# Kernel tuning notes

Hardware: AMD Instinct MI355X
Metric: run time of the kernel (lower is better)

Reference implementation:

```python
import jax, jax.numpy as jnp
import numpy as np

N, C, E = 4096, 128, 10          # nodes, channels, element types
LMAX = 2
NI = (LMAX + 1) ** 2             # 9 spherical components of node_feats
K = {1: 4, 2: 12, 3: 30}         # number of CG paths per correlation order
DIMS = [2 * L + 1 for L in range(LMAX + 1)]  # output irrep dims [1,3,5]


def setup_inputs() -> dict:
    key = jax.random.key(0)
    ks = iter(jax.random.split(key, 64))
    inp = {}
    inp["node_feats"] = jax.random.normal(next(ks), (N, C, NI), jnp.float32)
    inp["sc"] = jax.random.normal(next(ks), (N, C * sum(DIMS)), jnp.float32)
    z = jax.random.randint(next(ks), (N,), 0, E)
    inp["node_attrs"] = jax.nn.one_hot(z, E, dtype=jnp.float32)
    for L, d in enumerate(DIMS):
        # U tensors: fixed Clebsch-Gordan-structured constants (stand-in values,
        # correct shapes/contraction pattern of MACE's U_matrix buffers).
        inp[f"U3_L{L}"] = jax.random.normal(next(ks), (d, NI, NI, NI, K[3]), jnp.float32) * 0.05
        inp[f"U2_L{L}"] = jax.random.normal(next(ks), (d, NI, NI, K[2]), jnp.float32) * 0.05
        inp[f"U1_L{L}"] = jax.random.normal(next(ks), (d, NI, K[1]), jnp.float32) * 0.05
        # Element-dependent path weights [num_elements, k, channels]
        inp[f"W3_L{L}"] = jax.random.normal(next(ks), (E, K[3], C), jnp.float32) / np.sqrt(K[3])
        inp[f"W2_L{L}"] = jax.random.normal(next(ks), (E, K[2], C), jnp.float32) / np.sqrt(K[2])
        inp[f"W1_L{L}"] = jax.random.normal(next(ks), (E, K[1], C), jnp.float32) / np.sqrt(K[1])
        # o3.Linear channel-mixing weight for this irrep
        inp[f"lin_L{L}"] = jax.random.normal(next(ks), (C, C), jnp.float32)
    return inp


def _contract(x, y, U3, U2, U1, W3, W2, W1):
    """MACE symmetric contraction (correlation=3) for one output irrep.
    x: [b,c,n] node feats, y: [b,e] one-hot element attrs.
    Recursive einsum structure from mace.modules.symmetric_contraction.Contraction."""
    out = jnp.einsum('dijnk,ekc,bcn,be->bcdij', U3, W3, x, y)
    c2 = jnp.einsum('dijk,ekc,be->bcdij', U2, W2, y) + out
    out = jnp.einsum('bcdij,bcj->bcdi', c2, x)
    c1 = jnp.einsum('dik,ekc,be->bcdi', U1, W1, y) + out
    return jnp.einsum('bcdi,bci->bcd', c1, x)  # [b,c,d]


def reference(node_feats, sc, node_attrs,
              U3_L0, U2_L0, U1_L0, W3_L0, W2_L0, W1_L0, lin_L0,
              U3_L1, U2_L1, U1_L1, W3_L1, W2_L1, W1_L1, lin_L1,
              U3_L2, U2_L2, U1_L2, W3_L2, W2_L2, W1_L2, lin_L2):
    Us = [(U3_L0, U2_L0, U1_L0), (U3_L1, U2_L1, U1_L1), (U3_L2, U2_L2, U1_L2)]
    Ws = [(W3_L0, W2_L0, W1_L0), (W3_L1, W2_L1, W1_L1), (W3_L2, W2_L2, W1_L2)]
    lins = [lin_L0, lin_L1, lin_L2]
    c = node_feats.shape[1]
    norm = jnp.asarray(1.0 / np.sqrt(c), node_feats.dtype)
    outs = []
    for (u3, u2, u1), (w3, w2, w1), lw in zip(Us, Ws, lins):
        o = _contract(node_feats, node_attrs, u3, u2, u1, w3, w2, w1)  # [b,c,d]
        o = jnp.einsum('bcd,cf->bfd', o, lw) * norm                    # o3.Linear mix
        outs.append(o.reshape(o.shape[0], -1))
    return jnp.concatenate(outs, axis=-1) + sc
```

## Files before the change

kernel.cpp:

```cpp
#include <hip/hip_runtime.h>

#define NNODES 4096
#define NCH    128
#define NE     10
#define PADN   4736
#define NCHUNK 74
#define TSTRIDE 2048
#define DGSTRIDE 672


struct MTab { unsigned short v[220]; };
static constexpr MTab make_mtab() {
    MTab t{};
    int m = 0;
    for (int i = 0; i < 9; ++i) {
        t.v[m++] = (unsigned short)((1 << 12) | (i << 8) | (i << 4) | i);
        for (int j = i; j < 9; ++j) {
            t.v[m++] = (unsigned short)((2 << 12) | (i << 8) | (j << 4) | j);
            for (int n = j; n < 9; ++n)
                t.v[m++] = (unsigned short)((3 << 12) | (i << 8) | (j << 4) | n);
        }
    }
    return t;
}
__constant__ MTab c_mtab = make_mtab();

__global__ __launch_bounds__(1024) void k_prep(
    const float* __restrict__ attrs,
    const float* __restrict__ U3_0, const float* __restrict__ U3_1, const float* __restrict__ U3_2,
    const float* __restrict__ W3_0, const float* __restrict__ W3_1, const float* __restrict__ W3_2,
    const float* __restrict__ U2_0, const float* __restrict__ U2_1, const float* __restrict__ U2_2,
    const float* __restrict__ W2_0, const float* __restrict__ W2_1, const float* __restrict__ W2_2,
    const float* __restrict__ U1_0, const float* __restrict__ U1_1, const float* __restrict__ U1_2,
    const float* __restrict__ W1_0, const float* __restrict__ W1_1, const float* __restrict__ W1_2,
    int* __restrict__ list, int* __restrict__ chunkinfo,
    float* __restrict__ wcat, float* __restrict__ Usym)
{
    int bid = blockIdx.x, t = threadIdx.x;
    if (bid == 0) {
        __shared__ int hist[NE], cur[NE], base[NE + 1], cbase[NE + 1];
        if (t < NE) { hist[t] = 0; cur[t] = 0; }
        __syncthreads();
        int mye[4];
#pragma unroll
        for (int k = 0; k < 4; ++k) {
            int b = k * 1024 + t;
            const float* y = attrs + (size_t)b * NE;
            int e = 0;
#pragma unroll
            for (int u = 0; u < NE; ++u) if (y[u] > 0.5f) e = u;
            mye[k] = e;
            atomicAdd(&hist[e], 1);
        }
        for (int i = t; i < PADN; i += 1024) list[i] = -1;
        __syncthreads();
        if (t == 0) {
            int off = 0, goff = 0;
            for (int e = 0; e < NE; ++e) {
                base[e] = off; cbase[e] = goff;
                int nc = (hist[e] + 63) >> 6;
                off += nc * 64; goff += nc;
            }
            base[NE] = off; cbase[NE] = goff;
        }
        __syncthreads();
        if (t < 80) {
            int info = -1;
            if (t < cbase[NE]) {
                int e = 0;
                while (!(t >= cbase[e] && t < cbase[e + 1])) ++e;
                int k = t - cbase[e];
                int valid = hist[e] - k * 64; if (valid > 64) valid = 64;
                info = (base[e] + k * 64) | (valid << 16) | (e << 24);
            }
            chunkinfo[t] = info;
        } else if (t < 91) {
            chunkinfo[t] = cbase[t - 80];
        }
#pragma unroll
        for (int k = 0; k < 4; ++k) {
            int e = mye[k];
            int pos = atomicAdd(&cur[e], 1);
            list[base[e] + pos] = k * 1024 + t;
        }
    } else if (bid <= 10) {
        int e = bid - 1;
#pragma unroll 1
        for (int L = 0; L < 3; ++L) {
            const float* W1 = (L == 0) ? W1_0 : (L == 1) ? W1_1 : W1_2;
            const float* W2 = (L == 0) ? W2_0 : (L == 1) ? W2_1 : W2_2;
            const float* W3 = (L == 0) ? W3_0 : (L == 1) ? W3_1 : W3_2;
            for (int it = t; it < 48 * 128; it += 1024) {
                int c = it & 127, k = it >> 7;
                float v = 0.0f;
                if (k < 4)       v = W1[((size_t)e * 4 + k) * 128 + c];
                else if (k < 16) v = W2[((size_t)e * 12 + (k - 4)) * 128 + c];
                else if (k < 46) v = W3[((size_t)e * 30 + (k - 16)) * 128 + c];
                wcat[(((size_t)L * NE + e) * 48 + k) * 128 + c] = v;
            }
        }
    } else {
        int D = bid - 11;
        const float *U3, *U2, *U1; int dloc;
        if (D == 0)      { U3 = U3_0; U2 = U2_0; U1 = U1_0; dloc = 0; }
        else if (D < 4)  { U3 = U3_1; U2 = U2_1; U1 = U1_1; dloc = D - 1; }
        else             { U3 = U3_2; U2 = U2_2; U1 = U1_2; dloc = D - 4; }
        for (int it = t; it < 219 * 48; it += 1024) {
            int m = it / 48, k = it - m * 48;
            unsigned mv = c_mtab.v[m];
            int kind = mv >> 12, i = (mv >> 8) & 15, j = (mv >> 4) & 15, n = mv & 15;
            float v = 0.0f;
            if (kind == 1) {
                if (k < 4) v = U1[(size_t)(dloc * 9 + i) * 4 + k];
            } else if (kind == 2) {
                if (k >= 4 && k < 16) {
                    int kk = k - 4;
                    v = U2[(size_t)(dloc * 81 + i * 9 + j) * 12 + kk];
                    if (i != j) v += U2[(size_t)(dloc * 81 + j * 9 + i) * 12 + kk];
                }
            } else {
                if (k >= 16 && k < 46) {
                    int kk = k - 16;
                    v = U3[((size_t)dloc * 729 + i * 81 + j * 9 + n) * 30 + kk];
                    if (i == j) {
                        if (j != n)
                            v += U3[((size_t)dloc * 729 + i * 81 + n * 9 + i) * 30 + kk]
                               + U3[((size_t)dloc * 729 + n * 81 + i * 9 + i) * 30 + kk];
                    } else if (j == n) {
                        v += U3[((size_t)dloc * 729 + j * 81 + i * 9 + j) * 30 + kk]
                           + U3[((size_t)dloc * 729 + j * 81 + j * 9 + i) * 30 + kk];
                    } else {
                        v += U3[((size_t)dloc * 729 + i * 81 + n * 9 + j) * 30 + kk]
                           + U3[((size_t)dloc * 729 + j * 81 + i * 9 + n) * 30 + kk]
                           + U3[((size_t)dloc * 729 + j * 81 + n * 9 + i) * 30 + kk]
                           + U3[((size_t)dloc * 729 + n * 81 + i * 9 + j) * 30 + kk]
                           + U3[((size_t)dloc * 729 + n * 81 + j * 9 + i) * 30 + kk];
                    }
                }
            }
            Usym[((size_t)D * 219 + m) * 48 + k] = v;
        }
    }
}

__global__ __launch_bounds__(256) void k_tab(
    const float* __restrict__ wcat, const float* __restrict__ Usym,
    float* __restrict__ Sws)
{
    int bid = blockIdx.x;
    int e = bid / 12, r = bid - e * 12;
    int dg = r >> 2, mq = r & 3;
    int t = threadIdx.x;
    int c = t & 127;
    int sub = __builtin_amdgcn_readfirstlane(t >> 7);
    int D0 = dg * 3;
    int LA = (D0 == 0) ? 0 : (D0 < 4 ? 1 : 2);
    int LB = (D0 + 1 < 4) ? 1 : 2;

    float wcA[48], wcB[48];
#pragma unroll
    for (int k = 0; k < 48; ++k) {
        wcA[k] = wcat[(((size_t)LA * NE + e) * 48 + k) * 128 + c];
        wcB[k] = wcat[(((size_t)LB * NE + e) * 48 + k) * 128 + c];
    }

    float* outp = Sws + ((size_t)e * NCH + c) * TSTRIDE + dg * DGSTRIDE;
    int m1 = mq * 55 + 55; if (m1 > 219) m1 = 219;
#pragma unroll 1
    for (int m = mq * 55 + sub; m < m1; m += 2) {
        unsigned mv = c_mtab.v[m];
        int kind = mv >> 12;
        const float* up0 = Usym + ((size_t)D0 * 219 + m) * 48;
        const float* up1 = up0 + 219 * 48;
        const float* up2 = up1 + 219 * 48;
        float a0 = 0.0f, a1 = 0.0f, a2 = 0.0f;
        if (kind == 1) {
#pragma unroll
            for (int k = 0; k < 4; ++k) {
                a0 = fmaf(up0[k], wcA[k], a0);
                a1 = fmaf(up1[k], wcB[k], a1);
                a2 = fmaf(up2[k], wcB[k], a2);
            }
        } else if (kind == 2) {
#pragma unroll
            for (int k = 4; k < 16; ++k) {
                a0 = fmaf(up0[k], wcA[k], a0);
                a1 = fmaf(up1[k], wcB[k], a1);
                a2 = fmaf(up2[k], wcB[k], a2);
            }
        } else {
#pragma unroll
            for (int k = 16; k < 46; ++k) {
                a0 = fmaf(up0[k], wcA[k], a0);
                a1 = fmaf(up1[k], wcB[k], a1);
                a2 = fmaf(up2[k], wcB[k], a2);
            }
        }
        outp[m * 3 + 0] = a0;
        outp[m * 3 + 1] = a1;
        outp[m * 3 + 2] = a2;
    }
}

template <int NB>
__device__ __forceinline__ void do_chunks(
    const float* __restrict__ tab, const float* __restrict__ nf,
    const int* __restrict__ list, const int* __restrict__ chunkinfo,
    float* __restrict__ prep, int c, int gi, int lane)
{
    int pos[NB];
    float x[NB][9];
#pragma unroll
    for (int u = 0; u < NB; ++u) {
        int info = __builtin_amdgcn_readfirstlane(chunkinfo[gi + u]);
        pos[u] = (info & 0xffff) + lane;
        int b = list[pos[u]];
        const float* xp = nf + ((size_t)(b < 0 ? 0 : b) * 128 + c) * 9;
#pragma unroll
        for (int n = 0; n < 9; ++n) x[u][n] = (b >= 0) ? xp[n] : 0.0f;
    }

#pragma unroll 1
    for (int dg = 0; dg < 3; ++dg) {
        const float* s = tab + dg * DGSTRIDE;
        float a3[NB][3];
#pragma unroll
        for (int u = 0; u < NB; ++u)
#pragma unroll
            for (int d = 0; d < 3; ++d) a3[u][d] = 0.0f;
        int p = 0;
#pragma unroll
        for (int i = 0; i < 9; ++i) {
            float a2[NB][3];
#pragma unroll
            for (int d = 0; d < 3; ++d) {
                float tv = s[p + d];
#pragma unroll
                for (int u = 0; u < NB; ++u) a2[u][d] = tv;
            }
            p += 3;
#pragma unroll
            for (int j = i; j < 9; ++j) {
                float a1[NB][3];
#pragma unroll
                for (int d = 0; d < 3; ++d) {
                    float tv = s[p + d];
#pragma unroll
                    for (int u = 0; u < NB; ++u) a1[u][d] = tv;
                }
                p += 3;
#pragma unroll
                for (int n = j; n < 9; ++n) {
#pragma unroll
                    for (int d = 0; d < 3; ++d) {
                        float tv = s[p + d];
#pragma unroll
                        for (int u = 0; u < NB; ++u)
                            a1[u][d] = fmaf(tv, x[u][n], a1[u][d]);
                    }
                    p += 3;
                }
#pragma unroll
                for (int u = 0; u < NB; ++u)
#pragma unroll
                    for (int d = 0; d < 3; ++d)
                        a2[u][d] = fmaf(a1[u][d], x[u][j], a2[u][d]);
            }
#pragma unroll
            for (int u = 0; u < NB; ++u)
#pragma unroll
                for (int d = 0; d < 3; ++d)
                    a3[u][d] = fmaf(a2[u][d], x[u][i], a3[u][d]);
        }
#pragma unroll
        for (int u = 0; u < NB; ++u)
#pragma unroll
            for (int d = 0; d < 3; ++d)
                prep[(size_t)(dg * 3 + d) * PADN + pos[u]] = a3[u][d];
    }
}

__global__ __launch_bounds__(256) void k_main(
    const float* __restrict__ nf, const int* __restrict__ list,
    const int* __restrict__ chunkinfo, const float* __restrict__ Sws,
    float* __restrict__ pre)
{
    __shared__ __align__(16) float tab[TSTRIDE];
    int c = blockIdx.x, e = blockIdx.y;
    int t = threadIdx.x;
    int w = t >> 6, lane = t & 63;
    int cb0 = chunkinfo[80 + e], cb1 = chunkinfo[81 + e];
    if (cb0 >= cb1) return;

    {
        const float4* src = (const float4*)(Sws + ((size_t)e * NCH + c) * TSTRIDE);
        float4* dst = (float4*)tab;
        dst[t] = src[t];
        dst[t + 256] = src[t + 256];
    }
    __syncthreads();

    float* prep = pre + (size_t)c * 9 * PADN;

#pragma unroll 1
    for (int gi = cb0 + 2 * w; gi < cb1; gi += 8) {
        if (gi + 1 < cb1)
            do_chunks<2>(tab, nf, list, chunkinfo, prep, c, gi, lane);
        else
            do_chunks<1>(tab, nf, list, chunkinfo, prep, c, gi, lane);
    }
}

__global__ __launch_bounds__(256) void k_mix(
    const float* __restrict__ pre, const int* __restrict__ chunkinfo,
    const float* __restrict__ lin0, const float* __restrict__ lin1,
    const float* __restrict__ lin2, float* __restrict__ mixed)
{
    __shared__ __align__(16) float pt[128 * 64];
    int bid = blockIdx.x;
    int nt = bid >> 1;
    int fbase = (bid & 1) * 64;
    int n0 = nt * 64;
    int D = nt / NCHUNK;
    int g = nt - D * NCHUNK;
    if (chunkinfo[g] == -1) return;
    const float* lin = (D == 0) ? lin0 : (D < 4 ? lin1 : lin2);
    int t = threadIdx.x;

    {
        int q4 = (t & 15) * 4;
        int cb = t >> 4;
#pragma unroll
        for (int k = 0; k < 8; ++k) {
            int c = cb + k * 16;
            float4 v = *(const float4*)&pre[(size_t)c * 9 * PADN + n0 + q4];
            *(float4*)&pt[c * 64 + q4] = v;
        }
    }
    __syncthreads();

    int tq = t & 63;
    int f0 = fbase + __builtin_amdgcn_readfirstlane(t >> 6) * 16;
    float acc[16];
#pragma unroll
    for (int f = 0; f < 16; ++f) acc[f] = 0.0f;

#pragma unroll 4
    for (int c = 0; c < 128; ++c) {
        float pv = pt[c * 64 + tq];
        const float* lr = lin + c * 128 + f0;
#pragma unroll
        for (int f = 0; f < 16; ++f)
            acc[f] = fmaf(pv, lr[f], acc[f]);
    }

    const float nrm = 0.08838834764831845f;
#pragma unroll
    for (int f = 0; f < 16; ++f)
        mixed[(size_t)(f0 + f) * 9 * PADN + n0 + tq] = acc[f] * nrm;
}

__global__ __launch_bounds__(256) void k_out(
    const float* __restrict__ mixed, const int* __restrict__ list,
    const int* __restrict__ chunkinfo, const float* __restrict__ sc,
    float* __restrict__ out)
{
    __shared__ float tr[64 * 73];
    int fc = blockIdx.x, g = blockIdx.y;
    if (chunkinfo[g] == -1) return;
    int t = threadIdx.x;
    int fbase = fc * 8;
    int tf = t >> 6, tq = t & 63;

#pragma unroll
    for (int k = 0; k < 18; ++k) {
        int row = k * 4 + tf;
        int f = row / 9, D = row - f * 9;
        float v = mixed[((size_t)(fbase + f) * 9 + D) * PADN + g * 64 + tq];
        tr[tq * 73 + row] = v;
    }
    __syncthreads();

#pragma unroll 1
    for (int k = 0; k < 18; ++k) {
        int idx = k * 256 + t;
        int node = idx / 72, col = idx - node * 72;
        int b = list[g * 64 + node];
        if (b < 0) continue;
        int row, gcol;
        if (col < 8)       { row = col * 9;                       gcol = fbase + col; }
        else if (col < 32) { int u = col - 8;  int f = u / 3, dl = u - f * 3;
                             row = f * 9 + 1 + dl;                gcol = 128 + fbase * 3 + u; }
        else               { int u = col - 32; int f = u / 5, dl = u - f * 5;
                             row = f * 9 + 4 + dl;                gcol = 512 + fbase * 5 + u; }
        out[(size_t)b * 1152 + gcol] = tr[node * 73 + row] + sc[(size_t)b * 1152 + gcol];
    }
}

extern "C" void kernel_launch(void* const* d_in, const int* in_sizes, int n_in,
                              void* d_out, int out_size, void* d_ws, size_t ws_size,
                              hipStream_t stream)
{
    const float* nf    = (const float*)d_in[0];
    const float* sc    = (const float*)d_in[1];
    const float* attrs = (const float*)d_in[2];
    const float *U3s[3], *U2s[3], *U1s[3], *W3s[3], *W2s[3], *W1s[3], *lins[3];
    for (int L = 0; L < 3; ++L) {
        const int o = 3 + 7 * L;
        U3s[L]  = (const float*)d_in[o + 0];
        U2s[L]  = (const float*)d_in[o + 1];
        U1s[L]  = (const float*)d_in[o + 2];
        W3s[L]  = (const float*)d_in[o + 3];
        W2s[L]  = (const float*)d_in[o + 4];
        W1s[L]  = (const float*)d_in[o + 5];
        lins[L] = (const float*)d_in[o + 6];
    }

    float* wsf     = (float*)d_ws;
    int* chunkinfo = (int*)d_ws;
    int* list      = chunkinfo + 96;
    float* Sws   = wsf + 4864;
    float* pre   = Sws + (size_t)NE * NCH * TSTRIDE;
    float* mixed = pre + (size_t)NCH * 9 * PADN;
    float* wcat  = mixed + (size_t)NCH * 9 * PADN;
    float* Usym  = wcat + (size_t)3 * NE * 48 * 128;

    k_prep<<<20, 1024, 0, stream>>>(attrs,
                                    U3s[0], U3s[1], U3s[2], W3s[0], W3s[1], W3s[2],
                                    U2s[0], U2s[1], U2s[2], W2s[0], W2s[1], W2s[2],
                                    U1s[0], U1s[1], U1s[2], W1s[0], W1s[1], W1s[2],
                                    list, chunkinfo, wcat, Usym);
    k_tab<<<120, 256, 0, stream>>>(wcat, Usym, Sws);
    k_main<<<dim3(128, 10), 256, 0, stream>>>(nf, list, chunkinfo, Sws, pre);
    k_mix<<<1332, 256, 0, stream>>>(pre, chunkinfo, lins[0], lins[1], lins[2], mixed);
    k_out<<<dim3(16, NCHUNK), 256, 0, stream>>>(mixed, list, chunkinfo, sc, (float*)d_out);
}
```

Baseline: 255.2 us.

## Coalesce k_tab output via LDS transpose and replace atomic bucketing with ballot scans

k_tab now stages its per-channel results in a padded shared-memory tile and writes them to the table with lane-contiguous stores, where before each thread scattered strided stores by channel. The grid is doubled to 240 blocks, each covering 28 m-entries instead of 55, to add parallelism. In k_prep, the shared-memory atomic histogram and slot assignment are replaced with wave ballots, popcounts and a shuffle prefix scan, which removes atomic contention and gives a deterministic node order. The costs are extra LDS usage, a barrier, and reloading wcat in twice as many blocks.

```diff
diff --git a/kernel.cpp b/kernel.cpp
--- a/kernel.cpp
+++ b/kernel.cpp
@@ -38,9 +38,12 @@
 {
     int bid = blockIdx.x, t = threadIdx.x;
     if (bid == 0) {
-        __shared__ int hist[NE], cur[NE], base[NE + 1], cbase[NE + 1];
-        if (t < NE) { hist[t] = 0; cur[t] = 0; }
-        __syncthreads();
+        __shared__ int cnt[64][NE];
+        __shared__ int pfx[64][NE];
+        __shared__ int tot[NE];
+        __shared__ int base[NE + 1], cbase[NE + 1];
+        int w = t >> 6, lane = t & 63;
+        unsigned long long lmask = (1ull << lane) - 1ull;
         int mye[4];
 #pragma unroll
         for (int k = 0; k < 4; ++k) {
@@ -50,15 +53,32 @@
 #pragma unroll
             for (int u = 0; u < NE; ++u) if (y[u] > 0.5f) e = u;
             mye[k] = e;
-            atomicAdd(&hist[e], 1);
+#pragma unroll
+            for (int u = 0; u < NE; ++u) {
+                unsigned long long mb = __ballot(e == u);
+                if (lane == 0) cnt[w * 4 + k][u] = __popcll(mb);
+            }
         }
         for (int i = t; i < PADN; i += 1024) list[i] = -1;
+        __syncthreads();
+        if (t < 640) {
+            int e = t >> 6, wi = t & 63;
+            int v = cnt[wi][e];
+            int inc = v;
+#pragma unroll
+            for (int d = 1; d < 64; d <<= 1) {
+                int o = __shfl_up(inc, d, 64);
+                if (wi >= d) inc += o;
+            }
+            pfx[wi][e] = inc - v;
+            if (wi == 63) tot[e] = inc;
+        }
         __syncthreads();
         if (t == 0) {
             int off = 0, goff = 0;
             for (int e = 0; e < NE; ++e) {
                 base[e] = off; cbase[e] = goff;
-                int nc = (hist[e] + 63) >> 6;
+                int nc = (tot[e] + 63) >> 6;
                 off += nc * 64; goff += nc;
             }
             base[NE] = off; cbase[NE] = goff;
@@ -70,7 +90,7 @@
                 int e = 0;
                 while (!(t >= cbase[e] && t < cbase[e + 1])) ++e;
                 int k = t - cbase[e];
-                int valid = hist[e] - k * 64; if (valid > 64) valid = 64;
+                int valid = tot[e] - k * 64; if (valid > 64) valid = 64;
                 info = (base[e] + k * 64) | (valid << 16) | (e << 24);
             }
             chunkinfo[t] = info;
@@ -80,8 +100,14 @@
 #pragma unroll
         for (int k = 0; k < 4; ++k) {
             int e = mye[k];
-            int pos = atomicAdd(&cur[e], 1);
-            list[base[e] + pos] = k * 1024 + t;
+#pragma unroll
+            for (int u = 0; u < NE; ++u) {
+                unsigned long long mb = __ballot(e == u);
+                if (e == u) {
+                    int pos = base[u] + pfx[w * 4 + k][u] + __popcll(mb & lmask);
+                    list[pos] = k * 1024 + t;
+                }
+            }
         }
     } else if (bid <= 10) {
         int e = bid - 1;
@@ -147,9 +173,11 @@
     const float* __restrict__ wcat, const float* __restrict__ Usym,
     float* __restrict__ Sws)
 {
+    __shared__ __align__(16) float tile[84 * 129];
     int bid = blockIdx.x;
-    int e = bid / 12, r = bid - e * 12;
-    int dg = r >> 2, mq = r & 3;
+    int e = bid / 24, r0 = bid - e * 24;
+    int dg = r0 >> 3, mh = r0 & 7;
+    int m0 = mh * 28, m1 = m0 + 28; if (m1 > 219) m1 = 219;
     int t = threadIdx.x;
     int c = t & 127;
     int sub = __builtin_amdgcn_readfirstlane(t >> 7);
@@ -164,10 +192,8 @@
         wcB[k] = wcat[(((size_t)LB * NE + e) * 48 + k) * 128 + c];
     }
 
-    float* outp = Sws + ((size_t)e * NCH + c) * TSTRIDE + dg * DGSTRIDE;
-    int m1 = mq * 55 + 55; if (m1 > 219) m1 = 219;
-#pragma unroll 1
-    for (int m = mq * 55 + sub; m < m1; m += 2) {
+#pragma unroll 1
+    for (int m = m0 + sub; m < m1; m += 2) {
         unsigned mv = c_mtab.v[m];
         int kind = mv >> 12;
         const float* up0 = Usym + ((size_t)D0 * 219 + m) * 48;
@@ -196,9 +222,22 @@
                 a2 = fmaf(up2[k], wcB[k], a2);
             }
         }
-        outp[m * 3 + 0] = a0;
-        outp[m * 3 + 1] = a1;
-        outp[m * 3 + 2] = a2;
+        int rr = (m - m0) * 3;
+        tile[(rr + 0) * 129 + c] = a0;
+        tile[(rr + 1) * 129 + c] = a1;
+        tile[(rr + 2) * 129 + c] = a2;
+    }
+    __syncthreads();
+
+    int w = t >> 6, lane = t & 63;
+    int nrows = (m1 - m0) * 3;
+#pragma unroll 1
+    for (int cc = 0; cc < 32; ++cc) {
+        int co = w * 32 + cc;
+        float* op = Sws + ((size_t)e * NCH + co) * TSTRIDE + dg * DGSTRIDE + m0 * 3;
+#pragma unroll
+        for (int rr = lane; rr < 84; rr += 64)
+            if (rr < nrows) op[rr] = tile[rr * 129 + co];
     }
 }
 
@@ -430,7 +469,7 @@
                                     U2s[0], U2s[1], U2s[2], W2s[0], W2s[1], W2s[2],
                                     U1s[0], U1s[1], U1s[2], W1s[0], W1s[1], W1s[2],
                                     list, chunkinfo, wcat, Usym);
-    k_tab<<<120, 256, 0, stream>>>(wcat, Usym, Sws);
+    k_tab<<<240, 256, 0, stream>>>(wcat, Usym, Sws);
     k_main<<<dim3(128, 10), 256, 0, stream>>>(nf, list, chunkinfo, Sws, pre);
     k_mix<<<1332, 256, 0, stream>>>(pre, chunkinfo, lins[0], lins[1], lins[2], mixed);
     k_out<<<dim3(16, NCHUNK), 256, 0, stream>>>(mixed, list, chunkinfo, sc, (float*)d_out);
```

Result: faster. 241.7 us (median of 3 runs) (-5.3%).
